# Kernel tuning notes

Hardware: AMD Instinct MI355X
Metric: run time of the kernel (lower is better)

The kernel has to match this reference:

```python
import jax, jax.numpy as jnp
import numpy as np

DIM = 4
ORDER = 7  # order+1 = 8 Legendre polys per coordinate; features = 8**4 = 4096


def legendre_all(x, order):
    """Evaluate P_0..P_order at x (any shape) via Bonnet recurrence.
    Returns array of shape x.shape + (order+1,)."""
    p_prev = jnp.ones_like(x)  # P_0
    if order == 0:
        return p_prev[..., None]
    p_cur = x  # P_1
    polys = [p_prev, p_cur]
    for n in range(1, order):
        # (n+1) P_{n+1} = (2n+1) x P_n - n P_{n-1}
        p_next = ((2.0 * n + 1.0) * x * p_cur - float(n) * p_prev) / (n + 1.0)
        polys.append(p_next)
        p_prev, p_cur = p_cur, p_next
    return jnp.stack(polys, axis=-1)


def setup_inputs() -> dict:
    key = jax.random.key(0)
    k1, k2, k3 = jax.random.split(key, 3)
    N = 65536
    num = (ORDER + 1) ** DIM
    x = jax.random.uniform(k1, (N, DIM), dtype=jnp.float32)
    W = jax.random.normal(k2, (1, num), dtype=jnp.float32) * (1.0 / np.sqrt(num))
    b = jax.random.normal(k3, (1,), dtype=jnp.float32) * 0.01
    return {"x": x, "W": W, "b": b}


def reference(x, W, b):
    N = x.shape[0]
    # Legendre basis per coordinate: [N, DIM, ORDER+1]
    leg = legendre_all(x, ORDER)
    # Batched cartesian-product of basis values across the DIM axes.
    # torch.cartesian_prod varies the FIRST tensor slowest, so we expand
    # left-to-right: feat[n, i0*K + i1*... ] = prod_d leg[n, d, i_d].
    feat = leg[:, 0, :]  # [N, ORDER+1]
    for d in range(1, DIM):
        feat = (feat[:, :, None] * leg[:, d, :][:, None, :]).reshape(N, -1)
    # Final linear projection to scalar: [N, num] @ [num, 1] + b
    return feat @ W.T + b
```

## Files before the change

kernel.cpp:

```cpp
#include <hip/hip_runtime.h>
#include <hip/hip_bf16.h>


typedef short short8 __attribute__((ext_vector_type(8)));
typedef float floatx4 __attribute__((ext_vector_type(4)));

static __device__ inline unsigned short f2bs(float f) {
    return __builtin_bit_cast(unsigned short, __float2bfloat16(f));
}
static __device__ inline unsigned pk(float a, float b) {
    return (unsigned)f2bs(a) | ((unsigned)f2bs(b) << 16);
}

__global__ __launch_bounds__(256, 4) void mvpoly3(
    const float* __restrict__ x,
    const float* __restrict__ W,
    const float* __restrict__ bias,
    float* __restrict__ out,
    int N)
{
    __shared__ uint4 Wb[64 * 8];
    __shared__ float Gt[4][64 * 21];

    const int tid  = threadIdx.x;
    const int wid  = tid >> 6;
    const int lane = tid & 63;
    const int l15  = lane & 15;
    const int l4   = lane >> 4;

    {
        const int c  = tid >> 2;
        const int j0 = (tid & 3) * 16;
        const float4* ws = reinterpret_cast<const float4*>(W + c * 64 + j0);
        float4 w0 = ws[0], w1 = ws[1], w2 = ws[2], w3 = ws[3];
        uint4 ch0, ch1;
        ch0.x = pk(w0.x, w0.y); ch0.y = pk(w0.z, w0.w);
        ch0.z = pk(w1.x, w1.y); ch0.w = pk(w1.z, w1.w);
        ch1.x = pk(w2.x, w2.y); ch1.y = pk(w2.z, w2.w);
        ch1.z = pk(w3.x, w3.y); ch1.w = pk(w3.z, w3.w);
        const int sw = c & 7;
        Wb[c * 8 + (((j0 >> 3) + 0) ^ sw)] = ch0;
        Wb[c * 8 + (((j0 >> 3) + 1) ^ sw)] = ch1;
    }

    const int pbase = blockIdx.x * 64 + wid * 16;
    int p = pbase + l15;
    if (p >= N) p = N - 1;
    const float4 xv = reinterpret_cast<const float4*>(x)[p];

    float p0[8], p1[8], p2[8], p3[8];
    p0[0] = p1[0] = p2[0] = p3[0] = 1.f;
    p0[1] = xv.x; p1[1] = xv.y; p2[1] = xv.z; p3[1] = xv.w;
    #pragma unroll
    for (int k = 1; k < 7; ++k) {
        const float a = (2.f * k + 1.f) / (float)(k + 1);
        const float c = (float)k / (float)(k + 1);
        p0[k + 1] = a * xv.x * p0[k] - c * p0[k - 1];
        p1[k + 1] = a * xv.y * p1[k] - c * p1[k - 1];
        p2[k + 1] = a * xv.z * p2[k] - c * p2[k - 1];
        p3[k + 1] = a * xv.w * p3[k] - c * p3[k - 1];
    }

    const float s2a = (l4 == 0) ? p2[0] : (l4 == 1) ? p2[1] : (l4 == 2) ? p2[2] : p2[3];
    const float s2b = (l4 == 0) ? p2[4] : (l4 == 1) ? p2[5] : (l4 == 2) ? p2[6] : p2[7];
    uint4 fa0, fa1;
    fa0.x = pk(s2a * p3[0], s2a * p3[1]); fa0.y = pk(s2a * p3[2], s2a * p3[3]);
    fa0.z = pk(s2a * p3[4], s2a * p3[5]); fa0.w = pk(s2a * p3[6], s2a * p3[7]);
    fa1.x = pk(s2b * p3[0], s2b * p3[1]); fa1.y = pk(s2b * p3[2], s2b * p3[3]);
    fa1.z = pk(s2b * p3[4], s2b * p3[5]); fa1.w = pk(s2b * p3[6], s2b * p3[7]);
    const short8 af0 = __builtin_bit_cast(short8, fa0);
    const short8 af1 = __builtin_bit_cast(short8, fa1);

    __syncthreads();

    floatx4 acc[4];
    #pragma unroll
    for (int nt = 0; nt < 4; ++nt) acc[nt] = floatx4{0.f, 0.f, 0.f, 0.f};

    #pragma unroll
    for (int nt = 0; nt < 4; ++nt) {
        const int c = nt * 16 + l15;
        const short8 bf0 = *reinterpret_cast<const short8*>(&Wb[c * 8 + ((0 * 4 + l4) ^ (c & 7))]);
        const short8 bf1 = *reinterpret_cast<const short8*>(&Wb[c * 8 + ((1 * 4 + l4) ^ (c & 7))]);
        acc[nt] = __builtin_amdgcn_mfma_f32_16x16x32_bf16(af0, bf0, acc[nt], 0, 0, 0);
        acc[nt] = __builtin_amdgcn_mfma_f32_16x16x32_bf16(af1, bf1, acc[nt], 0, 0, 0);
    }

    float* gt = Gt[wid];
    #pragma unroll
    for (int nt = 0; nt < 4; ++nt) {
        #pragma unroll
        for (int q = 0; q < 4; ++q) {
            gt[(nt * 16 + l15) * 21 + (l4 * 4 + q)] = acc[nt][q];
        }
    }

    const float s0a = (l4 == 0) ? p0[0] : (l4 == 1) ? p0[2] : (l4 == 2) ? p0[4] : p0[6];
    const float s0b = (l4 == 0) ? p0[1] : (l4 == 1) ? p0[3] : (l4 == 2) ? p0[5] : p0[7];

    float part = 0.f;
    #pragma unroll
    for (int cc = 0; cc < 16; ++cc) {
        const float g  = gt[(l4 * 16 + cc) * 21 + l15];
        const float f0 = (cc < 8) ? s0a : s0b;
        part = fmaf(g * p1[cc & 7], f0, part);
    }
    part += __shfl_xor(part, 16, 64);
    part += __shfl_xor(part, 32, 64);

    if (l4 == 0) {
        const int po = pbase + l15;
        if (po < N) out[po] = part + bias[0];
    }
}

extern "C" void kernel_launch(void* const* d_in, const int* in_sizes, int n_in,
                              void* d_out, int out_size, void* d_ws, size_t ws_size,
                              hipStream_t stream) {
    const float* x = (const float*)d_in[0];
    const float* W = (const float*)d_in[1];
    const float* b = (const float*)d_in[2];
    float* out = (float*)d_out;

    const int N = in_sizes[0] / 4;
    const int grid = (N + 63) / 64;

    hipLaunchKernelGGL(mvpoly3, dim3(grid), dim3(256), 0, stream,
                       x, W, b, out, N);
}
```

Baseline: 9.723 us.

## Swap MFMA operands so output layout matches points, removing LDS transpose

Makes W the A operand and point features the B operand of the MFMA. Each lane then holds its own point's results across channels, so the final contraction with the first two Legendre factors happens in registers. This removes the per-wave shared-memory transpose buffer and its stores and loads, and cuts LDS use, which may allow more resident blocks. The lane-to-channel mapping now has to line up exactly with the MFMA output layout.

```diff
diff --git a/kernel.cpp b/kernel.cpp
--- a/kernel.cpp
+++ b/kernel.cpp
@@ -12,7 +12,7 @@
     return (unsigned)f2bs(a) | ((unsigned)f2bs(b) << 16);
 }
 
-__global__ __launch_bounds__(256, 4) void mvpoly3(
+__global__ __launch_bounds__(256, 4) void mvpoly4(
     const float* __restrict__ x,
     const float* __restrict__ W,
     const float* __restrict__ bias,
@@ -20,7 +20,6 @@
     int N)
 {
     __shared__ uint4 Wb[64 * 8];
-    __shared__ float Gt[4][64 * 21];
 
     const int tid  = threadIdx.x;
     const int wid  = tid >> 6;
@@ -63,47 +62,41 @@
 
     const float s2a = (l4 == 0) ? p2[0] : (l4 == 1) ? p2[1] : (l4 == 2) ? p2[2] : p2[3];
     const float s2b = (l4 == 0) ? p2[4] : (l4 == 1) ? p2[5] : (l4 == 2) ? p2[6] : p2[7];
-    uint4 fa0, fa1;
-    fa0.x = pk(s2a * p3[0], s2a * p3[1]); fa0.y = pk(s2a * p3[2], s2a * p3[3]);
-    fa0.z = pk(s2a * p3[4], s2a * p3[5]); fa0.w = pk(s2a * p3[6], s2a * p3[7]);
-    fa1.x = pk(s2b * p3[0], s2b * p3[1]); fa1.y = pk(s2b * p3[2], s2b * p3[3]);
-    fa1.z = pk(s2b * p3[4], s2b * p3[5]); fa1.w = pk(s2b * p3[6], s2b * p3[7]);
-    const short8 af0 = __builtin_bit_cast(short8, fa0);
-    const short8 af1 = __builtin_bit_cast(short8, fa1);
+    uint4 fb0, fb1;
+    fb0.x = pk(s2a * p3[0], s2a * p3[1]); fb0.y = pk(s2a * p3[2], s2a * p3[3]);
+    fb0.z = pk(s2a * p3[4], s2a * p3[5]); fb0.w = pk(s2a * p3[6], s2a * p3[7]);
+    fb1.x = pk(s2b * p3[0], s2b * p3[1]); fb1.y = pk(s2b * p3[2], s2b * p3[3]);
+    fb1.z = pk(s2b * p3[4], s2b * p3[5]); fb1.w = pk(s2b * p3[6], s2b * p3[7]);
+    const short8 bf0 = __builtin_bit_cast(short8, fb0);
+    const short8 bf1 = __builtin_bit_cast(short8, fb1);
 
     __syncthreads();
 
     floatx4 acc[4];
     #pragma unroll
-    for (int nt = 0; nt < 4; ++nt) acc[nt] = floatx4{0.f, 0.f, 0.f, 0.f};
-
-    #pragma unroll
-    for (int nt = 0; nt < 4; ++nt) {
-        const int c = nt * 16 + l15;
-        const short8 bf0 = *reinterpret_cast<const short8*>(&Wb[c * 8 + ((0 * 4 + l4) ^ (c & 7))]);
-        const short8 bf1 = *reinterpret_cast<const short8*>(&Wb[c * 8 + ((1 * 4 + l4) ^ (c & 7))]);
-        acc[nt] = __builtin_amdgcn_mfma_f32_16x16x32_bf16(af0, bf0, acc[nt], 0, 0, 0);
-        acc[nt] = __builtin_amdgcn_mfma_f32_16x16x32_bf16(af1, bf1, acc[nt], 0, 0, 0);
+    for (int mt = 0; mt < 4; ++mt) {
+        const int c  = mt * 16 + l15;
+        const int sw = c & 7;
+        const short8 wf0 = *reinterpret_cast<const short8*>(&Wb[c * 8 + ((0 + l4) ^ sw)]);
+        const short8 wf1 = *reinterpret_cast<const short8*>(&Wb[c * 8 + ((4 + l4) ^ sw)]);
+        floatx4 a = floatx4{0.f, 0.f, 0.f, 0.f};
+        a = __builtin_amdgcn_mfma_f32_16x16x32_bf16(wf0, bf0, a, 0, 0, 0);
+        a = __builtin_amdgcn_mfma_f32_16x16x32_bf16(wf1, bf1, a, 0, 0, 0);
+        acc[mt] = a;
     }
 
-    float* gt = Gt[wid];
+    float p1s[4];
     #pragma unroll
-    for (int nt = 0; nt < 4; ++nt) {
-        #pragma unroll
-        for (int q = 0; q < 4; ++q) {
-            gt[(nt * 16 + l15) * 21 + (l4 * 4 + q)] = acc[nt][q];
-        }
-    }
-
-    const float s0a = (l4 == 0) ? p0[0] : (l4 == 1) ? p0[2] : (l4 == 2) ? p0[4] : p0[6];
-    const float s0b = (l4 == 0) ? p0[1] : (l4 == 1) ? p0[3] : (l4 == 2) ? p0[5] : p0[7];
+    for (int q = 0; q < 4; ++q) p1s[q] = (l4 & 1) ? p1[q + 4] : p1[q];
 
     float part = 0.f;
     #pragma unroll
-    for (int cc = 0; cc < 16; ++cc) {
-        const float g  = gt[(l4 * 16 + cc) * 21 + l15];
-        const float f0 = (cc < 8) ? s0a : s0b;
-        part = fmaf(g * p1[cc & 7], f0, part);
+    for (int mt = 0; mt < 4; ++mt) {
+        const float f0 = (l4 >= 2) ? p0[mt * 2 + 1] : p0[mt * 2];
+        float inner = 0.f;
+        #pragma unroll
+        for (int q = 0; q < 4; ++q) inner = fmaf(acc[mt][q], p1s[q], inner);
+        part = fmaf(f0, inner, part);
     }
     part += __shfl_xor(part, 16, 64);
     part += __shfl_xor(part, 32, 64);
@@ -125,6 +118,6 @@
     const int N = in_sizes[0] / 4;
     const int grid = (N + 63) / 64;
 
-    hipLaunchKernelGGL(mvpoly3, dim3(grid), dim3(256), 0, stream,
+    hipLaunchKernelGGL(mvpoly4, dim3(grid), dim3(256), 0, stream,
                        x, W, b, out, N);
 }
```

Measured after the change: 34.69 us. +256.8%, slower.
